# Kernel tuning notes

Hardware: AMD Instinct MI355X
Metric: run time of the kernel (lower is better)

Reference implementation:

```python
import jax, jax.numpy as jnp
import numpy as np
import math

# Zero-indexed Fano plane lines: {i, i+1, i+3} mod 7
FANO_LINES = np.array([[0,1,3],[1,2,4],[2,3,5],[3,4,6],[4,5,0],[5,6,1],[6,0,2]])
WINDOW = 16  # local window hardcoded in create_expanded_mask

HIDDEN = 896
HEADS = 7
HEAD_DIM = HIDDEN // HEADS  # 128
B, T = 4, 2048


def fano_expanded_mask(T, causal):
    # line membership per head: [7, T] -> True where (j % 7) in line
    jm = np.arange(T) % 7
    line_hit = np.zeros((7, T), dtype=bool)
    for h in range(7):
        line_hit[h] = np.isin(jm, FANO_LINES[h])
    line_hit = jnp.asarray(line_hit)
    i = jnp.arange(T)[:, None]
    j = jnp.arange(T)[None, :]
    if causal:
        causal_m = j <= i                      # [T, T]
        local = (j >= i - WINDOW) & (j <= i)   # causal local window [i-16, i]
        mask = (line_hit[:, None, :] & causal_m[None]) | local[None]
    else:
        local = (j >= i - WINDOW) & (j <= i + WINDOW)
        mask = line_hit[:, None, :] | local[None]
    return mask  # [7, T, T], True = attend


def setup_inputs() -> dict:
    key = jax.random.key(0)
    kx, kq, kk, kv, ko = jax.random.split(key, 5)
    s = 1.0 / math.sqrt(HIDDEN)
    return {
        "x": jax.random.normal(kx, (B, T, HIDDEN), dtype=jnp.float32),
        "Wq": jax.random.normal(kq, (HEADS, HIDDEN, HEAD_DIM), dtype=jnp.float32) * s,
        "Wk": jax.random.normal(kk, (HEADS, HIDDEN, HEAD_DIM), dtype=jnp.float32) * s,
        "Wv": jax.random.normal(kv, (HEADS, HIDDEN, HEAD_DIM), dtype=jnp.float32) * s,
        "Wo": jax.random.normal(ko, (HIDDEN, HIDDEN), dtype=jnp.float32) * s,
        "is_causal": 1,
    }


def reference(x, Wq, Wk, Wv, Wo, is_causal):
    Bx, Tx, H = x.shape
    d = Wq.shape[-1]
    scale = 1.0 / math.sqrt(d)
    # per-head projections (no bias): [7, B, T, d]
    q = jnp.einsum('bth,nhd->nbtd', x, Wq)
    k = jnp.einsum('bth,nhd->nbtd', x, Wk)
    v = jnp.einsum('bth,nhd->nbtd', x, Wv)
    mask = fano_expanded_mask(Tx, bool(is_causal))        # [7, T, T]
    attn = jnp.einsum('nbtd,nbsd->nbts', q, k) * scale    # [7, B, T, T]
    attn = jnp.where(mask[:, None], attn, -jnp.inf)
    attn = jax.nn.softmax(attn, axis=-1)                  # every row has j=i valid
    out = jnp.einsum('nbts,nbsd->nbtd', attn, v)          # [7, B, T, d]
    combined = out.transpose(1, 2, 0, 3).reshape(Bx, Tx, H)  # concat heads
    return combined @ Wo.T
```

## Files before the change

kernel.cpp:

```cpp
#include <hip/hip_runtime.h>
#include <hip/hip_bf16.h>

#define HIDDEN 896
#define HEADS 7
#define HDIM 128
#define BB 4
#define TT 2048
#define MTOT (BB*TT)

#define KSP 132
#define VSP 68
#define PSP 68

#define SCP 896

typedef short bf16x8 __attribute__((ext_vector_type(8)));
typedef float f32x4 __attribute__((ext_vector_type(4)));

__device__ __forceinline__ short f2bf(float f) {
    union { float f; unsigned u; } v; v.f = f;
    unsigned r = (v.u + 0x7FFF + ((v.u >> 16) & 1)) >> 16;
    return (short)r;
}

__device__ __forceinline__ void gll16(const short* g, short* l) {
    __builtin_amdgcn_global_load_lds(
        (const __attribute__((address_space(1))) unsigned int*)g,
        (__attribute__((address_space(3))) unsigned int*)l, 16, 0, 0);
}

__device__ __forceinline__ unsigned linemask(int h) {
    return ((0x0Bu << h) | (0x0Bu >> (7 - h))) & 0x7Fu;
}
__device__ __forceinline__ int linecnt(unsigned m, int X) {
    return (X / 7) * 3 + __popc(m & ((1u << (X % 7)) - 1u));
}

#define NB_CASTX (MTOT * HIDDEN / 1024)
#define NB_CASTWO (HIDDEN * HIDDEN / 1024)
#define NB_TRANS (28 * 4 * 21)
__global__ __launch_bounds__(256) void prep_fused(
    const float* __restrict__ x, const float* __restrict__ Wo,
    const float* __restrict__ Wq, const float* __restrict__ Wk,
    const float* __restrict__ Wv,
    short* __restrict__ xb, short* __restrict__ Wob, short* __restrict__ Wt)
{
    __shared__ float tile[32][33];
    const int bid = blockIdx.x;
    if (bid < NB_CASTX) {
        int base = (bid * 256 + threadIdx.x) * 4;
        float4 v = *(const float4*)(x + base);
        short4 o;
        o.x = f2bf(v.x); o.y = f2bf(v.y); o.z = f2bf(v.z); o.w = f2bf(v.w);
        *(short4*)(xb + base) = o;
    } else if (bid < NB_CASTX + NB_CASTWO) {
        int base = ((bid - NB_CASTX) * 256 + threadIdx.x) * 4;
        float4 v = *(const float4*)(Wo + base);
        short4 o;
        o.x = f2bf(v.x); o.y = f2bf(v.y); o.z = f2bf(v.z); o.w = f2bf(v.w);
        *(short4*)(Wob + base) = o;
    } else {
        int t = bid - NB_CASTX - NB_CASTWO;
        const int z = t / 112;
        const int rem = t % 112;
        const int bx = rem % 28, by = rem / 28;
        const int type = z / 7, head = z % 7;
        const float* src = (type == 0 ? Wq : (type == 1 ? Wk : Wv)) + head * (HIDDEN * HDIM);
        short* dst = Wt + (size_t)z * (HDIM * HIDDEN);
        const int r0 = bx * 32, c0 = by * 32;
        const int tx = threadIdx.x & 31, ty = threadIdx.x >> 5;
        for (int i = 0; i < 4; i++)
            tile[ty * 4 + i][tx] = src[(r0 + ty * 4 + i) * HDIM + c0 + tx];
        __syncthreads();
        for (int i = 0; i < 4; i++)
            dst[(c0 + ty * 4 + i) * HIDDEN + r0 + tx] = f2bf(tile[tx][ty * 4 + i]);
    }
}

__global__ __launch_bounds__(256) void qkv_gemm(
    const short* __restrict__ xb, const short* __restrict__ Wt,
    short* __restrict__ Q, short* __restrict__ Kk, short* __restrict__ Vt)
{
    __shared__ short Ash[2][128 * 32];
    __shared__ short Bsh[2][128 * 32];
    const int z = blockIdx.x;
    const int m0 = blockIdx.y * 128;
    const int head = z % 7, type = z / 7;
    const short* Wz = Wt + (size_t)z * (HDIM * HIDDEN);

    const int tid = threadIdx.x;
    const int wave = tid >> 6, lane = tid & 63;
    const int quad = lane >> 4, l16 = lane & 15;
    const int wm = (wave >> 1) * 64, wn = (wave & 1) * 64;

    f32x4 acc[4][4] = {};

    const int r0 = tid >> 2, cc0 = (tid & 3) * 8;
    const int r1 = r0 + 64;
    const short* asrc0 = xb + (size_t)(m0 + r0) * HIDDEN + cc0;
    const short* asrc1 = xb + (size_t)(m0 + r1) * HIDDEN + cc0;
    const short* bsrc0 = Wz + (size_t)r0 * HIDDEN + cc0;
    const short* bsrc1 = Wz + (size_t)r1 * HIDDEN + cc0;

    for (int k0 = 0; k0 < HIDDEN; k0 += 64) {
        __syncthreads();
        for (int s = 0; s < 2; s++) {
            gll16(asrc0 + k0 + s * 32, &Ash[s][wave * 512]);
            gll16(asrc1 + k0 + s * 32, &Ash[s][2048 + wave * 512]);
            gll16(bsrc0 + k0 + s * 32, &Bsh[s][wave * 512]);
            gll16(bsrc1 + k0 + s * 32, &Bsh[s][2048 + wave * 512]);
        }
        __syncthreads();
        for (int s = 0; s < 2; s++) {
            bf16x8 af[4], bfr[4];
            for (int mi = 0; mi < 4; mi++)
                af[mi] = *(const bf16x8*)(&Ash[s][(wm + mi * 16 + l16) * 32 + quad * 8]);
            for (int ni = 0; ni < 4; ni++)
                bfr[ni] = *(const bf16x8*)(&Bsh[s][(wn + ni * 16 + l16) * 32 + quad * 8]);
            for (int mi = 0; mi < 4; mi++)
                for (int ni = 0; ni < 4; ni++)
                    acc[mi][ni] = __builtin_amdgcn_mfma_f32_16x16x32_bf16(af[mi], bfr[ni], acc[mi][ni], 0, 0, 0);
        }
    }

    const size_t base = (size_t)head * (MTOT * HDIM);
    if (type == 0) {
        const float qs = 0.08838834764831845f * 1.4426950408889634f;
        for (int mi = 0; mi < 4; mi++)
            for (int ni = 0; ni < 4; ni++)
                for (int r = 0; r < 4; r++) {
                    int m = m0 + wm + mi * 16 + quad * 4 + r;
                    int n = wn + ni * 16 + l16;
                    Q[base + (size_t)m * HDIM + n] = f2bf(acc[mi][ni][r] * qs);
                }
    } else if (type == 1) {
        for (int mi = 0; mi < 4; mi++)
            for (int ni = 0; ni < 4; ni++)
                for (int r = 0; r < 4; r++) {
                    int m = m0 + wm + mi * 16 + quad * 4 + r;
                    int n = wn + ni * 16 + l16;
                    Kk[base + (size_t)m * HDIM + n] = f2bf(acc[mi][ni][r]);
                }
    } else {
        for (int mi = 0; mi < 4; mi++)
            for (int ni = 0; ni < 4; ni++) {
                int m = m0 + wm + mi * 16 + quad * 4;
                int bb = m >> 11, t = m & 2047;
                int n = wn + ni * 16 + l16;
                short4 o;
                o.x = f2bf(acc[mi][ni][0]); o.y = f2bf(acc[mi][ni][1]);
                o.z = f2bf(acc[mi][ni][2]); o.w = f2bf(acc[mi][ni][3]);
                *(short4*)(Vt + base + (size_t)bb * (HDIM * TT) + (size_t)n * TT + t) = o;
            }
    }
}

__global__ __launch_bounds__(256) void compact_k(const short* __restrict__ K,
                                                 short* __restrict__ Kc)
{
    const int hb = blockIdx.x, h = hb >> 2, b = hb & 3;
    const unsigned m = linemask(h);
    const int c_tot = 876 + __popc(m & 0xFu);
    const int o0 = __ffs(m) - 1;
    const unsigned m1 = m & (m - 1);
    const int o1 = __ffs(m1) - 1;
    const unsigned m2 = m1 & (m1 - 1);
    const int o2 = __ffs(m2) - 1;
    const int r = blockIdx.y * 32 + (threadIdx.x >> 3);
    const int c = (threadIdx.x & 7) * 16;
    short* dst = Kc + ((size_t)hb * SCP + r) * HDIM + c;
    if (r < c_tot) {
        int g = r / 3, id = r - g * 3;
        int s = g * 7 + (id == 0 ? o0 : (id == 1 ? o1 : o2));
        const short* src = K + (size_t)(h * MTOT + b * TT + s) * HDIM + c;
        *(bf16x8*)dst = *(const bf16x8*)src;
        *(bf16x8*)(dst + 8) = *(const bf16x8*)(src + 8);
    } else {
        bf16x8 z = {};
        *(bf16x8*)dst = z;
        *(bf16x8*)(dst + 8) = z;
    }
}

__global__ __launch_bounds__(256) void compact_v(const short* __restrict__ Vt,
                                                 short* __restrict__ Vc)
{
    const int hb = blockIdx.x, h = hb >> 2, b = hb & 3;
    const int d = blockIdx.y;
    const unsigned m = linemask(h);
    const int c_tot = 876 + __popc(m & 0xFu);
    const int o0 = __ffs(m) - 1;
    const unsigned m1 = m & (m - 1);
    const int o1 = __ffs(m1) - 1;
    const unsigned m2 = m1 & (m1 - 1);
    const int o2 = __ffs(m2) - 1;
    const short* src = Vt + (size_t)h * MTOT * HDIM + (size_t)b * HDIM * TT + (size_t)d * TT;
    short* dst = Vc + ((size_t)hb * HDIM + d) * SCP;
    for (int sp = threadIdx.x * 4; sp < SCP; sp += 1024) {
        short4 o;
        short* po = (short*)&o;
        for (int j = 0; j < 4; j++) {
            int spp = sp + j;
            short v = 0;
            if (spp < c_tot) {
                int g = spp / 3, id = spp - g * 3;
                int s = g * 7 + (id == 0 ? o0 : (id == 1 ? o1 : o2));
                v = src[s];
            }
            po[j] = v;
        }
        *(short4*)(dst + sp) = o;
    }
}

__global__ __launch_bounds__(256) void fano_attn(
    const short* __restrict__ Q, const short* __restrict__ K, const short* __restrict__ Vt,
    const short* __restrict__ Kc, const short* __restrict__ Vc,
    short* __restrict__ Ocat, const int* __restrict__ iscp)
{
    __shared__ short Ks[64 * KSP];
    __shared__ short Vs[128 * VSP];
    __shared__ short Ps[4][32 * PSP];

    const int causal = *iscp;
    const int mlin = blockIdx.y + 4 * blockIdx.z;
    const int qt = (causal && mlin >= 16) ? ((int)gridDim.x - 1 - blockIdx.x)
                                          : (int)blockIdx.x;
    const int q0 = qt * 128;
    const int b = blockIdx.y, h = blockIdx.z;
    const int hb = h * 4 + b;
    const int tid = threadIdx.x, wave = tid >> 6, lane = tid & 63;
    const int quad = lane >> 4, l16 = lane & 15;
    const int iw = q0 + wave * 32;

    const short* Qb = Q + (size_t)(h * MTOT + b * TT + q0) * HDIM;
    const short* Kb = K + (size_t)(h * MTOT + b * TT) * HDIM;
    const short* Vb = Vt + (size_t)h * MTOT * HDIM + (size_t)b * HDIM * TT;
    const short* Kcb = Kc + (size_t)hb * SCP * HDIM;
    const short* Vcb = Vc + (size_t)hb * HDIM * SCP;

    bf16x8 qf[2][4];
    for (int g = 0; g < 2; g++)
        for (int ks = 0; ks < 4; ks++)
            qf[g][ks] = *(const bf16x8*)(Qb + (size_t)(wave * 32 + g * 16 + l16) * HDIM + ks * 32 + quad * 8);

    f32x4 oacc[2][8] = {};
    f32x4 lacc[2] = {};
    int irow[2][4];
    for (int g = 0; g < 2; g++)
        for (int r = 0; r < 4; r++)
            irow[g][r] = q0 + wave * 32 + g * 16 + quad * 4 + r;

    const bf16x8 vones = {0x3F80, 0x3F80, 0x3F80, 0x3F80, 0x3F80, 0x3F80, 0x3F80, 0x3F80};

    int krow[4], kcol[4], vrow[4], vcol[4];
    for (int i = 0; i < 4; i++) {
        int c = tid + i * 256;
        krow[i] = c >> 4; kcol[i] = (c & 15) * 8;
        vrow[i] = c >> 3; vcol[i] = (c & 7) * 8;
    }

    const unsigned m_h = linemask(h);
    const int c_tot = 876 + __popc(m_h & 0xFu);
    const int sB0 = (causal && q0 >= 64) ? (q0 - 64) : 0;
    const int sB1 = causal ? (q0 + 128) : (q0 + 192 < TT ? q0 + 192 : TT);
    const int cA = linecnt(m_h, sB0);
    const int cC0 = causal ? c_tot : linecnt(m_h, sB1);
    const int l16h = (l16 - h + 7) % 7;

    short* Pw = &Ps[wave][0];

    const int nph = causal ? 2 : 3;
    for (int p = 0; p < nph; p++) {
        const short *Kp, *Vp;
        int vstr, t0, t1, c0v = 0, c1v = 0;
        if (p == 0)      { Kp = Kcb; Vp = Vcb; vstr = SCP; t0 = 0;        t1 = (cA + 63) >> 6;    c0v = 0;   c1v = cA; }
        else if (p == 1) { Kp = Kb;  Vp = Vb;  vstr = TT;  t0 = sB0 >> 6; t1 = sB1 >> 6; }
        else             { Kp = Kcb; Vp = Vcb; vstr = SCP; t0 = cC0 >> 6; t1 = (c_tot + 63) >> 6; c0v = cC0; c1v = c_tot; }
        if (t0 >= t1) continue;
        const bool comp = (p != 1);
        int s0q = sB0 % 7;

        bf16x8 kreg[4], vreg[4];
        {
            const int si = t0 * 64;
            for (int i = 0; i < 4; i++) {
                kreg[i] = *(const bf16x8*)(Kp + (size_t)(si + krow[i]) * HDIM + kcol[i]);
                vreg[i] = *(const bf16x8*)(Vp + (size_t)vrow[i] * vstr + si + vcol[i]);
            }
        }

        for (int t = t0; t < t1; t++) {
            const int s0 = t * 64;
            __syncthreads();
            for (int i = 0; i < 4; i++) {
                *(bf16x8*)(Ks + krow[i] * KSP + kcol[i]) = kreg[i];
                *(bf16x8*)(Vs + vrow[i] * VSP + vcol[i]) = vreg[i];
            }
            __syncthreads();

            int tn = t + 1; if (tn >= t1) tn = t0;
            const int sn = tn * 64;
            for (int i = 0; i < 4; i++) {
                kreg[i] = *(const bf16x8*)(Kp + (size_t)(sn + krow[i]) * HDIM + kcol[i]);
                vreg[i] = *(const bf16x8*)(Vp + (size_t)vrow[i] * vstr + sn + vcol[i]);
            }

            f32x4 sacc[2][4] = {};
            for (int ni = 0; ni < 4; ni++)
                for (int ks = 0; ks < 4; ks++) {
                    bf16x8 bk = *(const bf16x8*)(Ks + (ni * 16 + l16) * KSP + ks * 32 + quad * 8);
                    sacc[0][ni] = __builtin_amdgcn_mfma_f32_16x16x32_bf16(qf[0][ks], bk, sacc[0][ni], 0, 0, 0);
                    sacc[1][ni] = __builtin_amdgcn_mfma_f32_16x16x32_bf16(qf[1][ks], bk, sacc[1][ni], 0, 0, 0);
                }

            if (comp) {
                for (int ni = 0; ni < 4; ni++) {
                    int scol = s0 + ni * 16 + l16;
                    bool ok = (scol >= c0v) & (scol < c1v);
                    for (int g = 0; g < 2; g++)
                        for (int r = 0; r < 4; r++)
                            sacc[g][ni][r] = ok ? exp2f(sacc[g][ni][r]) : 0.0f;
                }
            } else {
                int d7b = l16h + s0q; if (d7b >= 7) d7b -= 7;
                for (int ni = 0; ni < 4; ni++) {
                    int d7 = d7b + 2 * ni; if (d7 >= 7) d7 -= 7;
                    bool line = (0x0B >> d7) & 1;
                    int s = s0 + ni * 16 + l16;
                    for (int g = 0; g < 2; g++)
                        for (int r = 0; r < 4; r++) {
                            int i = irow[g][r];
                            bool ok = causal ? ((s <= i) & (line | (s >= i - 16)))
                                             : (line | ((s >= i - 16) & (s <= i + 16)));
                            sacc[g][ni][r] = ok ? exp2f(sacc[g][ni][r]) : 0.0f;
                        }
                }
                s0q++; if (s0q == 7) s0q = 0;
            }

            for (int g = 0; g < 2; g++)
                for (int ni = 0; ni < 4; ni++)
                    for (int r = 0; r < 4; r++)
                        Pw[(g * 16 + quad * 4 + r) * PSP + ni * 16 + l16] = f2bf(sacc[g][ni][r]);

            for (int ks2 = 0; ks2 < 2; ks2++) {
                bf16x8 ap0 = *(const bf16x8*)(Pw + l16 * PSP + ks2 * 32 + quad * 8);
                bf16x8 ap1 = *(const bf16x8*)(Pw + (16 + l16) * PSP + ks2 * 32 + quad * 8);
                lacc[0] = __builtin_amdgcn_mfma_f32_16x16x32_bf16(ap0, vones, lacc[0], 0, 0, 0);
                lacc[1] = __builtin_amdgcn_mfma_f32_16x16x32_bf16(ap1, vones, lacc[1], 0, 0, 0);
                for (int nj = 0; nj < 8; nj++) {
                    bf16x8 bv = *(const bf16x8*)(Vs + (nj * 16 + l16) * VSP + ks2 * 32 + quad * 8);
                    oacc[0][nj] = __builtin_amdgcn_mfma_f32_16x16x32_bf16(ap0, bv, oacc[0][nj], 0, 0, 0);
                    oacc[1][nj] = __builtin_amdgcn_mfma_f32_16x16x32_bf16(ap1, bv, oacc[1][nj], 0, 0, 0);
                }
            }
        }
    }

    short* Obase = Ocat + (size_t)(b * TT) * HIDDEN + h * HDIM;
    for (int g = 0; g < 2; g++) {
        float inv[4];
        for (int r = 0; r < 4; r++) inv[r] = 1.0f / lacc[g][r];
        for (int nj = 0; nj < 8; nj++)
            for (int r = 0; r < 4; r++)
                Obase[(size_t)irow[g][r] * HIDDEN + nj * 16 + l16] = f2bf(oacc[g][nj][r] * inv[r]);
    }
}

__global__ __launch_bounds__(256) void out_gemm(
    const short* __restrict__ A, const short* __restrict__ Bt, float* __restrict__ out)
{
    __shared__ short Ash[2][128 * 32];
    __shared__ short Bsh[2][128 * 32];
    const int n0 = blockIdx.x * 128;
    const int m0 = blockIdx.y * 128;

    const int tid = threadIdx.x;
    const int wave = tid >> 6, lane = tid & 63;
    const int quad = lane >> 4, l16 = lane & 15;
    const int wm = (wave >> 1) * 64, wn = (wave & 1) * 64;

    f32x4 acc[4][4] = {};

    const int r0 = tid >> 2, cc0 = (tid & 3) * 8;
    const int r1 = r0 + 64;
    const short* asrc0 = A + (size_t)(m0 + r0) * HIDDEN + cc0;
    const short* asrc1 = A + (size_t)(m0 + r1) * HIDDEN + cc0;
    const short* bsrc0 = Bt + (size_t)(n0 + r0) * HIDDEN + cc0;
    const short* bsrc1 = Bt + (size_t)(n0 + r1) * HIDDEN + cc0;

    for (int k0 = 0; k0 < HIDDEN; k0 += 64) {
        __syncthreads();
        for (int s = 0; s < 2; s++) {
            gll16(asrc0 + k0 + s * 32, &Ash[s][wave * 512]);
            gll16(asrc1 + k0 + s * 32, &Ash[s][2048 + wave * 512]);
            gll16(bsrc0 + k0 + s * 32, &Bsh[s][wave * 512]);
            gll16(bsrc1 + k0 + s * 32, &Bsh[s][2048 + wave * 512]);
        }
        __syncthreads();
        for (int s = 0; s < 2; s++) {
            bf16x8 af[4], bfr[4];
            for (int mi = 0; mi < 4; mi++)
                af[mi] = *(const bf16x8*)(&Ash[s][(wm + mi * 16 + l16) * 32 + quad * 8]);
            for (int ni = 0; ni < 4; ni++)
                bfr[ni] = *(const bf16x8*)(&Bsh[s][(wn + ni * 16 + l16) * 32 + quad * 8]);
            for (int mi = 0; mi < 4; mi++)
                for (int ni = 0; ni < 4; ni++)
                    acc[mi][ni] = __builtin_amdgcn_mfma_f32_16x16x32_bf16(af[mi], bfr[ni], acc[mi][ni], 0, 0, 0);
        }
    }

    for (int mi = 0; mi < 4; mi++)
        for (int ni = 0; ni < 4; ni++)
            for (int r = 0; r < 4; r++) {
                int m = m0 + wm + mi * 16 + quad * 4 + r;
                int n = n0 + wn + ni * 16 + l16;
                out[(size_t)m * HIDDEN + n] = acc[mi][ni][r];
            }
}

extern "C" void kernel_launch(void* const* d_in, const int* in_sizes, int n_in,
                              void* d_out, int out_size, void* d_ws, size_t ws_size,
                              hipStream_t stream) {
    (void)in_sizes; (void)n_in; (void)out_size; (void)ws_size;
    const float* x  = (const float*)d_in[0];
    const float* Wq = (const float*)d_in[1];
    const float* Wk = (const float*)d_in[2];
    const float* Wv = (const float*)d_in[3];
    const float* Wo = (const float*)d_in[4];
    const int* iscp = (const int*)d_in[5];
    float* out = (float*)d_out;

    short* xb   = (short*)d_ws;
    short* Qb   = xb   + (size_t)MTOT * HIDDEN;
    short* Kb   = Qb   + (size_t)HEADS * MTOT * HDIM;
    short* Vtb  = Kb   + (size_t)HEADS * MTOT * HDIM;
    short* Ocat = Vtb  + (size_t)HEADS * MTOT * HDIM;
    short* Wt   = Ocat;
    short* Wob  = Ocat + (size_t)MTOT * HIDDEN;
    short* Kc   = xb;
    short* Vc   = Kc + (size_t)28 * SCP * HDIM;

    prep_fused<<<NB_CASTX + NB_CASTWO + NB_TRANS, 256, 0, stream>>>(
        x, Wo, Wq, Wk, Wv, xb, Wob, Wt);
    qkv_gemm<<<dim3(21, MTOT / 128), 256, 0, stream>>>(xb, Wt, Qb, Kb, Vtb);
    compact_k<<<dim3(28, SCP / 32), 256, 0, stream>>>(Kb, Kc);
    compact_v<<<dim3(28, HDIM), 256, 0, stream>>>(Vtb, Vc);
    fano_attn<<<dim3(TT / 128, BB, HEADS), 256, 0, stream>>>(Qb, Kb, Vtb, Kc, Vc, Ocat, iscp);
    out_gemm<<<dim3(HIDDEN / 128, MTOT / 128), 256, 0, stream>>>(Ocat, Wob, out);
}
```

Measured before the change: 321.3 us.

## Triple-buffer GEMM k-loop with async prefetch and XCD-aware block swizzle

Both the QKV and output GEMMs now use a three-slot LDS ring. The next k-tile's global-to-LDS loads are issued before computing the current tile, with a counted vmcnt wait and a single barrier per step instead of two syncthreads per 64-wide chunk. The grid is flattened to 1D and block indices are remapped so that consecutive blocks on each of the 8 XCDs share operand tiles, which should improve L2 reuse. The costs are more LDS per block, which could lower occupancy, and correctness now depends on the exact vmcnt accounting of the gll16 loads.

```diff
diff --git a/kernel.cpp b/kernel.cpp
--- a/kernel.cpp
+++ b/kernel.cpp
@@ -81,10 +81,12 @@
     const short* __restrict__ xb, const short* __restrict__ Wt,
     short* __restrict__ Q, short* __restrict__ Kk, short* __restrict__ Vt)
 {
-    __shared__ short Ash[2][128 * 32];
-    __shared__ short Bsh[2][128 * 32];
-    const int z = blockIdx.x;
-    const int m0 = blockIdx.y * 128;
+    __shared__ short Ash[3 * 128 * 32];
+    __shared__ short Bsh[3 * 128 * 32];
+    const int orig = blockIdx.x;
+    const int sblk = (orig & 7) * 168 + (orig >> 3);
+    const int z = sblk % 21;
+    const int m0 = (sblk / 21) * 128;
     const int head = z % 7, type = z / 7;
     const short* Wz = Wt + (size_t)z * (HDIM * HIDDEN);
 
@@ -102,25 +104,38 @@
     const short* bsrc0 = Wz + (size_t)r0 * HIDDEN + cc0;
     const short* bsrc1 = Wz + (size_t)r1 * HIDDEN + cc0;
 
-    for (int k0 = 0; k0 < HIDDEN; k0 += 64) {
-        __syncthreads();
-        for (int s = 0; s < 2; s++) {
-            gll16(asrc0 + k0 + s * 32, &Ash[s][wave * 512]);
-            gll16(asrc1 + k0 + s * 32, &Ash[s][2048 + wave * 512]);
-            gll16(bsrc0 + k0 + s * 32, &Bsh[s][wave * 512]);
-            gll16(bsrc1 + k0 + s * 32, &Bsh[s][2048 + wave * 512]);
+    auto STAGE = [&](int kt, int sel) {
+        const int ko = kt * 32;
+        short* ab = Ash + sel * 4096;
+        short* bb = Bsh + sel * 4096;
+        gll16(asrc0 + ko, ab + wave * 512);
+        gll16(asrc1 + ko, ab + 2048 + wave * 512);
+        gll16(bsrc0 + ko, bb + wave * 512);
+        gll16(bsrc1 + ko, bb + 2048 + wave * 512);
+    };
+
+    STAGE(0, 0);
+    const int NT = HIDDEN / 32;
+    for (int t = 0; t < NT; t++) {
+        const int sel = t % 3;
+        if (t + 1 < NT) {
+            STAGE(t + 1, (t + 1) % 3);
+            asm volatile("s_waitcnt vmcnt(4)" ::: "memory");
+        } else {
+            asm volatile("s_waitcnt vmcnt(0)" ::: "memory");
         }
-        __syncthreads();
-        for (int s = 0; s < 2; s++) {
-            bf16x8 af[4], bfr[4];
-            for (int mi = 0; mi < 4; mi++)
-                af[mi] = *(const bf16x8*)(&Ash[s][(wm + mi * 16 + l16) * 32 + quad * 8]);
+        __builtin_amdgcn_s_barrier();
+        __builtin_amdgcn_sched_barrier(0);
+        const short* ab = Ash + sel * 4096;
+        const short* bb = Bsh + sel * 4096;
+        bf16x8 af[4], bfr[4];
+        for (int mi = 0; mi < 4; mi++)
+            af[mi] = *(const bf16x8*)(ab + (wm + mi * 16 + l16) * 32 + quad * 8);
+        for (int ni = 0; ni < 4; ni++)
+            bfr[ni] = *(const bf16x8*)(bb + (wn + ni * 16 + l16) * 32 + quad * 8);
+        for (int mi = 0; mi < 4; mi++)
             for (int ni = 0; ni < 4; ni++)
-                bfr[ni] = *(const bf16x8*)(&Bsh[s][(wn + ni * 16 + l16) * 32 + quad * 8]);
-            for (int mi = 0; mi < 4; mi++)
-                for (int ni = 0; ni < 4; ni++)
-                    acc[mi][ni] = __builtin_amdgcn_mfma_f32_16x16x32_bf16(af[mi], bfr[ni], acc[mi][ni], 0, 0, 0);
-        }
+                acc[mi][ni] = __builtin_amdgcn_mfma_f32_16x16x32_bf16(af[mi], bfr[ni], acc[mi][ni], 0, 0, 0);
     }
 
     const size_t base = (size_t)head * (MTOT * HDIM);
@@ -145,12 +160,12 @@
         for (int mi = 0; mi < 4; mi++)
             for (int ni = 0; ni < 4; ni++) {
                 int m = m0 + wm + mi * 16 + quad * 4;
-                int bb = m >> 11, t = m & 2047;
+                int bb2 = m >> 11, t = m & 2047;
                 int n = wn + ni * 16 + l16;
                 short4 o;
                 o.x = f2bf(acc[mi][ni][0]); o.y = f2bf(acc[mi][ni][1]);
                 o.z = f2bf(acc[mi][ni][2]); o.w = f2bf(acc[mi][ni][3]);
-                *(short4*)(Vt + base + (size_t)bb * (HDIM * TT) + (size_t)n * TT + t) = o;
+                *(short4*)(Vt + base + (size_t)bb2 * (HDIM * TT) + (size_t)n * TT + t) = o;
             }
     }
 }
@@ -176,9 +191,9 @@
         *(bf16x8*)dst = *(const bf16x8*)src;
         *(bf16x8*)(dst + 8) = *(const bf16x8*)(src + 8);
     } else {
-        bf16x8 z = {};
-        *(bf16x8*)dst = z;
-        *(bf16x8*)(dst + 8) = z;
+        bf16x8 zz = {};
+        *(bf16x8*)dst = zz;
+        *(bf16x8*)(dst + 8) = zz;
     }
 }
 
@@ -371,10 +386,12 @@
 __global__ __launch_bounds__(256) void out_gemm(
     const short* __restrict__ A, const short* __restrict__ Bt, float* __restrict__ out)
 {
-    __shared__ short Ash[2][128 * 32];
-    __shared__ short Bsh[2][128 * 32];
-    const int n0 = blockIdx.x * 128;
-    const int m0 = blockIdx.y * 128;
+    __shared__ short Ash[3 * 128 * 32];
+    __shared__ short Bsh[3 * 128 * 32];
+    const int orig = blockIdx.x;
+    const int sblk = (orig & 7) * 56 + (orig >> 3);
+    const int n0 = (sblk % 7) * 128;
+    const int m0 = (sblk / 7) * 128;
 
     const int tid = threadIdx.x;
     const int wave = tid >> 6, lane = tid & 63;
@@ -390,25 +407,38 @@
     const short* bsrc0 = Bt + (size_t)(n0 + r0) * HIDDEN + cc0;
     const short* bsrc1 = Bt + (size_t)(n0 + r1) * HIDDEN + cc0;
 
-    for (int k0 = 0; k0 < HIDDEN; k0 += 64) {
-        __syncthreads();
-        for (int s = 0; s < 2; s++) {
-            gll16(asrc0 + k0 + s * 32, &Ash[s][wave * 512]);
-            gll16(asrc1 + k0 + s * 32, &Ash[s][2048 + wave * 512]);
-            gll16(bsrc0 + k0 + s * 32, &Bsh[s][wave * 512]);
-            gll16(bsrc1 + k0 + s * 32, &Bsh[s][2048 + wave * 512]);
+    auto STAGE = [&](int kt, int sel) {
+        const int ko = kt * 32;
+        short* ab = Ash + sel * 4096;
+        short* bb = Bsh + sel * 4096;
+        gll16(asrc0 + ko, ab + wave * 512);
+        gll16(asrc1 + ko, ab + 2048 + wave * 512);
+        gll16(bsrc0 + ko, bb + wave * 512);
+        gll16(bsrc1 + ko, bb + 2048 + wave * 512);
+    };
+
+    STAGE(0, 0);
+    const int NT = HIDDEN / 32;
+    for (int t = 0; t < NT; t++) {
+        const int sel = t % 3;
+        if (t + 1 < NT) {
+            STAGE(t + 1, (t + 1) % 3);
+            asm volatile("s_waitcnt vmcnt(4)" ::: "memory");
+        } else {
+            asm volatile("s_waitcnt vmcnt(0)" ::: "memory");
         }
-        __syncthreads();
-        for (int s = 0; s < 2; s++) {
-            bf16x8 af[4], bfr[4];
-            for (int mi = 0; mi < 4; mi++)
-                af[mi] = *(const bf16x8*)(&Ash[s][(wm + mi * 16 + l16) * 32 + quad * 8]);
+        __builtin_amdgcn_s_barrier();
+        __builtin_amdgcn_sched_barrier(0);
+        const short* ab = Ash + sel * 4096;
+        const short* bb = Bsh + sel * 4096;
+        bf16x8 af[4], bfr[4];
+        for (int mi = 0; mi < 4; mi++)
+            af[mi] = *(const bf16x8*)(ab + (wm + mi * 16 + l16) * 32 + quad * 8);
+        for (int ni = 0; ni < 4; ni++)
+            bfr[ni] = *(const bf16x8*)(bb + (wn + ni * 16 + l16) * 32 + quad * 8);
+        for (int mi = 0; mi < 4; mi++)
             for (int ni = 0; ni < 4; ni++)
-                bfr[ni] = *(const bf16x8*)(&Bsh[s][(wn + ni * 16 + l16) * 32 + quad * 8]);
-            for (int mi = 0; mi < 4; mi++)
-                for (int ni = 0; ni < 4; ni++)
-                    acc[mi][ni] = __builtin_amdgcn_mfma_f32_16x16x32_bf16(af[mi], bfr[ni], acc[mi][ni], 0, 0, 0);
-        }
+                acc[mi][ni] = __builtin_amdgcn_mfma_f32_16x16x32_bf16(af[mi], bfr[ni], acc[mi][ni], 0, 0, 0);
     }
 
     for (int mi = 0; mi < 4; mi++)
@@ -444,9 +474,9 @@
 
     prep_fused<<<NB_CASTX + NB_CASTWO + NB_TRANS, 256, 0, stream>>>(
         x, Wo, Wq, Wk, Wv, xb, Wob, Wt);
-    qkv_gemm<<<dim3(21, MTOT / 128), 256, 0, stream>>>(xb, Wt, Qb, Kb, Vtb);
+    qkv_gemm<<<21 * (MTOT / 128), 256, 0, stream>>>(xb, Wt, Qb, Kb, Vtb);
     compact_k<<<dim3(28, SCP / 32), 256, 0, stream>>>(Kb, Kc);
     compact_v<<<dim3(28, HDIM), 256, 0, stream>>>(Vtb, Vc);
     fano_attn<<<dim3(TT / 128, BB, HEADS), 256, 0, stream>>>(Qb, Kb, Vtb, Kc, Vc, Ocat, iscp);
-    out_gemm<<<dim3(HIDDEN / 128, MTOT / 128), 256, 0, stream>>>(Ocat, Wob, out);
-}
+    out_gemm<<<(HIDDEN / 128) * (MTOT / 128), 256, 0, stream>>>(Ocat, Wob, out);
+}
```

After: 282.1 us. 12.2% less time.
